# Kernel tuning notes

Hardware: AMD Instinct MI355X
Metric: run time of the kernel (lower is better)

The kernel has to match this reference:

```python
import jax, jax.numpy as jnp
import numpy as np

N_NODES = 100000
NEG_SLOPE = 0.01  # torch F.leaky_relu default


def sage_gcn_layer(feat, src, dst, W, b):
    # DGL SAGEConv, aggregator_type='gcn':
    #   h_i = fc_neigh((sum_{j->i} x_j + x_i) / (in_deg_i + 1))
    neigh_sum = jax.ops.segment_sum(feat[src], dst, num_segments=N_NODES)
    deg = jax.ops.segment_sum(jnp.ones((src.shape[0],), feat.dtype), dst,
                              num_segments=N_NODES)
    h = (neigh_sum + feat) / (deg + 1.0)[:, None]
    return h @ W + b


def setup_inputs() -> dict:
    key = jax.random.key(0)
    k_feat, k_e, k_w1, k_w2 = jax.random.split(key, 4)
    d_in, d_hid, d_out = 128, 128, 128
    E = 1600000
    feat = jax.random.normal(k_feat, (N_NODES, d_in), dtype=jnp.float32)
    edge_index = jax.random.randint(k_e, (2, E), 0, N_NODES, dtype=jnp.int64)
    W1 = jax.random.normal(k_w1, (d_in, d_hid), dtype=jnp.float32) / np.sqrt(d_in)
    b1 = jnp.zeros((d_hid,), jnp.float32)
    W2 = jax.random.normal(k_w2, (d_hid, d_out), dtype=jnp.float32) / np.sqrt(d_hid)
    b2 = jnp.zeros((d_out,), jnp.float32)
    return {"feat": feat, "edge_index": edge_index,
            "W1": W1, "b1": b1, "W2": W2, "b2": b2}


def reference(feat, edge_index, W1, b1, W2, b2):
    src, dst = edge_index[0], edge_index[1]
    h = sage_gcn_layer(feat, src, dst, W1, b1)
    h = jax.nn.leaky_relu(h, NEG_SLOPE)
    # dropout = 0 -> identity
    h = sage_gcn_layer(h, src, dst, W2, b2)
    return jax.nn.leaky_relu(h, NEG_SLOPE)
```

## Files before the change

kernel.cpp:

```cpp
#include <hip/hip_runtime.h>

#define NEG_SLOPE 0.01f
#define BSHIFT 8
#define BMASK 255
#define BMAX 512

typedef __attribute__((ext_vector_type(8))) short bf16x8;
typedef __attribute__((ext_vector_type(4))) float f32x4;
typedef __attribute__((ext_vector_type(2))) float f32x2;
typedef __attribute__((ext_vector_type(4))) unsigned u32x4;

static __device__ inline unsigned short f2b(float f) {
    unsigned u = __builtin_bit_cast(unsigned, f);
    return (unsigned short)((u + 0x7FFF + ((u >> 16) & 1)) >> 16);
}
static __device__ inline float b2f_lo(unsigned u) {
    return __builtin_bit_cast(float, u << 16);
}
static __device__ inline float b2f_hi(unsigned u) {
    return __builtin_bit_cast(float, u & 0xFFFF0000u);
}

__global__ __launch_bounds__(256) void cvt_feat(const float* __restrict__ x,
                                                unsigned short* __restrict__ xb,
                                                long long n) {
    long long i = ((long long)blockIdx.x * 256 + threadIdx.x) * 4;
    if (i < n) {
        float4 v = *(const float4*)(x + i);
        ushort4 o;
        o.x = f2b(v.x); o.y = f2b(v.y); o.z = f2b(v.z); o.w = f2b(v.w);
        *(ushort4*)(xb + i) = o;
    }
}

__global__ __launch_bounds__(256) void cvt_w(const float* __restrict__ W1,
                                             const float* __restrict__ W2,
                                             unsigned short* __restrict__ Wt1,
                                             unsigned short* __restrict__ Wt2,
                                             int* __restrict__ bcnt, int B) {
    int i = blockIdx.x * 256 + threadIdx.x;
    if (i < B) bcnt[i] = 0;
    int n = i & 127, k = i >> 7;
    Wt1[n * 128 + k] = f2b(W1[k * 128 + n]);
    Wt2[n * 128 + k] = f2b(W2[k * 128 + n]);
}

__global__ __launch_bounds__(256) void bhist_kernel(const int* __restrict__ dst,
                                                    int* __restrict__ bcnt,
                                                    int E, int B) {
    __shared__ int h[BMAX];
    for (int i = threadIdx.x; i < B; i += 256) h[i] = 0;
    __syncthreads();
    const int stride = gridDim.x * blockDim.x;
    for (int e = blockIdx.x * blockDim.x + threadIdx.x; e < E; e += stride)
        atomicAdd(&h[dst[e] >> BSHIFT], 1);
    __syncthreads();
    for (int i = threadIdx.x; i < B; i += 256)
        if (h[i]) atomicAdd(&bcnt[i], h[i]);
}

__global__ __launch_bounds__(512) void bscan_kernel(const int* __restrict__ bcnt,
                                                    int* __restrict__ bcursor,
                                                    int* __restrict__ bstart, int B) {
    __shared__ int sh[512];
    const int t = threadIdx.x;
    int v = (t < B) ? bcnt[t] : 0;
    sh[t] = v;
    __syncthreads();
    for (int d = 1; d < 512; d <<= 1) {
        int u = (t >= d) ? sh[t - d] : 0;
        __syncthreads();
        sh[t] += u;
        __syncthreads();
    }
    if (t < B) {
        int excl = sh[t] - v;
        bcursor[t] = excl;
        bstart[t] = excl;
    }
    if (t == B - 1) bstart[B] = sh[t];
}

__global__ __launch_bounds__(256) void bscatter_kernel(const int* __restrict__ src,
                                                       const int* __restrict__ dst,
                                                       int* __restrict__ bcursor,
                                                       unsigned* __restrict__ pairs,
                                                       int E, int B) {
    __shared__ int h[BMAX];
    __shared__ int base[BMAX];
    const int t = threadIdx.x;
    for (int i = t; i < B; i += 256) h[i] = 0;
    __syncthreads();
    const int chunk = (E + gridDim.x - 1) / gridDim.x;
    const int e0 = blockIdx.x * chunk;
    const int e1 = min(e0 + chunk, E);
    for (int e = e0 + t; e < e1; e += 256)
        atomicAdd(&h[dst[e] >> BSHIFT], 1);
    __syncthreads();
    for (int i = t; i < B; i += 256) {
        int c = h[i];
        base[i] = c ? atomicAdd(&bcursor[i], c) : 0;
    }
    __syncthreads();
    for (int i = t; i < B; i += 256) h[i] = base[i];
    __syncthreads();
    for (int e = e0 + t; e < e1; e += 256) {
        int d = dst[e];
        int pos = atomicAdd(&h[d >> BSHIFT], 1);
        pairs[pos] = (unsigned)src[e] | ((unsigned)(d & BMASK) << 24);
    }
}

__global__ __launch_bounds__(256) void bfinal_kernel(const unsigned* __restrict__ pairs,
                                                     const int* __restrict__ bstart,
                                                     int* __restrict__ offsets,
                                                     int* __restrict__ csr,
                                                     int N, int E) {
    __shared__ int h[256];
    __shared__ int cur[256];
    const int b = blockIdx.x;
    const int t = threadIdx.x;
    const int e0 = bstart[b], e1 = bstart[b + 1];
    h[t] = 0;
    __syncthreads();
    for (int e = e0 + t; e < e1; e += 256)
        atomicAdd(&h[pairs[e] >> 24], 1);
    __syncthreads();
    int v = h[t];
    for (int d = 1; d < 256; d <<= 1) {
        int u = (t >= d) ? h[t - d] : 0;
        __syncthreads();
        h[t] += u;
        __syncthreads();
    }
    const int base = e0 + (h[t] - v);
    const int node = (b << BSHIFT) + t;
    if (node < N) offsets[node] = base;
    if (b == (int)gridDim.x - 1 && t == 255) offsets[N] = E;
    cur[t] = base;
    __syncthreads();
    for (int e = e0 + t; e < e1; e += 256) {
        unsigned pr = pairs[e];
        int pos = atomicAdd(&cur[pr >> 24], 1);
        csr[pos] = (int)(pr & 0xFFFFFFu);
    }
}

static __device__ inline f32x2 up2(unsigned u) {
    return (f32x2){ b2f_lo(u), b2f_hi(u) };
}

#define GATHER(dst, off) \
    asm volatile("global_load_dwordx4 %0, %1, %2" : "=v"(dst) : "v"(off), "s"(xc))
#define ACCM(u, mk) do { \
    A0 += up2((u).x & (mk)); A1 += up2((u).y & (mk)); \
    A2 += up2((u).z & (mk)); A3 += up2((u).w & (mk)); } while (0)

__global__ __launch_bounds__(256) void aggregate_kernel(const unsigned short* __restrict__ xb,
                                                        const int* __restrict__ offsets,
                                                        const int* __restrict__ csr,
                                                        unsigned short* __restrict__ Hb,
                                                        int N) {
    const int node = (blockIdx.x * blockDim.x + threadIdx.x) >> 6;
    if (node >= N) return;
    const int lane = threadIdx.x & 63;
    const int g = lane >> 4;
    const unsigned poff = (unsigned)((lane & 15) << 4);
    const int start = offsets[node];
    const int end   = offsets[node + 1];
    const int deg   = end - start;
    const int rounds = deg >> 2;
    const int tailn  = deg & 3;
    const char* __restrict__ xc = (const char*)xb;

    const unsigned soff = ((unsigned)node << 8) | poff;
    u32x4 vs;
    GATHER(vs, soff);

    const int jmax = end - 1;
    unsigned o0, o1, o2, o3, o4, o5, o6, o7, ot;
#define CIDX(dsto, r) do { \
        int j = start + ((r) << 2) + g; j = j > jmax ? jmax : j; \
        int s = csr[j]; s = min(max(s, 0), N - 1); \
        dsto = ((unsigned)s << 8) | poff; } while (0)
    CIDX(o0, 0); CIDX(o1, 1); CIDX(o2, 2); CIDX(o3, 3);
    CIDX(o4, 4); CIDX(o5, 5); CIDX(o6, 6); CIDX(o7, 7);
    { int j = start + (rounds << 2) + g; j = j > jmax ? jmax : j;
      j = j < 0 ? 0 : j;
      int s = csr[j]; s = min(max(s, 0), N - 1);
      ot = ((unsigned)s << 8) | poff; }
#undef CIDX

    const unsigned m0 = rounds >= 1 ? ~0u : 0u;
    const unsigned m1 = rounds >= 2 ? ~0u : 0u;
    const unsigned m2 = rounds >= 3 ? ~0u : 0u;
    const unsigned m3 = rounds >= 4 ? ~0u : 0u;
    const unsigned m4 = rounds >= 5 ? ~0u : 0u;
    const unsigned m5 = rounds >= 6 ? ~0u : 0u;
    const unsigned m6 = rounds >= 7 ? ~0u : 0u;
    const unsigned m7 = rounds >= 8 ? ~0u : 0u;
    const unsigned mt = g < tailn ? ~0u : 0u;

    __builtin_amdgcn_sched_barrier(0);

    u32x4 v0, v1, v2, v3, v4, v5, v6, v7, vt;
    GATHER(v0, o0); GATHER(v1, o1); GATHER(v2, o2); GATHER(v3, o3);
    GATHER(v4, o4); GATHER(v5, o5); GATHER(v6, o6); GATHER(v7, o7);
    GATHER(vt, ot);
    asm volatile("s_waitcnt vmcnt(0)" ::: "memory");
    __builtin_amdgcn_sched_barrier(0);

    f32x2 A0 = {0.f, 0.f}, A1 = {0.f, 0.f}, A2 = {0.f, 0.f}, A3 = {0.f, 0.f};
    ACCM(v0, m0); ACCM(v1, m1); ACCM(v2, m2); ACCM(v3, m3);
    ACCM(v4, m4); ACCM(v5, m5); ACCM(v6, m6); ACCM(v7, m7);
    ACCM(vt, mt);
    for (int r = 8; r < rounds; ++r) {
        int s = csr[start + (r << 2) + g];
        s = min(max(s, 0), N - 1);
        u32x4 u = *(const u32x4*)(xc + (((unsigned)s << 8) | poff));
        ACCM(u, ~0u);
    }

    float a[8];
    a[0] = A0.x; a[1] = A0.y; a[2] = A1.x; a[3] = A1.y;
    a[4] = A2.x; a[5] = A2.y; a[6] = A3.x; a[7] = A3.y;
#pragma unroll
    for (int i = 0; i < 8; ++i) {
        a[i] += __shfl_xor(a[i], 16);
        a[i] += __shfl_xor(a[i], 32);
    }
    a[0] += b2f_lo(vs.x); a[1] += b2f_hi(vs.x);
    a[2] += b2f_lo(vs.y); a[3] += b2f_hi(vs.y);
    a[4] += b2f_lo(vs.z); a[5] += b2f_hi(vs.z);
    a[6] += b2f_lo(vs.w); a[7] += b2f_hi(vs.w);

    const float inv = 1.0f / (float)(deg + 1);
    if (g == 0) {
        uint4 o;
        o.x = (unsigned)f2b(a[0] * inv) | ((unsigned)f2b(a[1] * inv) << 16);
        o.y = (unsigned)f2b(a[2] * inv) | ((unsigned)f2b(a[3] * inv) << 16);
        o.z = (unsigned)f2b(a[4] * inv) | ((unsigned)f2b(a[5] * inv) << 16);
        o.w = (unsigned)f2b(a[6] * inv) | ((unsigned)f2b(a[7] * inv) << 16);
        *(uint4*)((char*)Hb + (((unsigned)node << 8) | poff)) = o;
    }
}

template <bool OUT_BF16>
__global__ __launch_bounds__(256) void gemm_mfma(const unsigned short* __restrict__ Hb,
                                                 const unsigned short* __restrict__ Wt,
                                                 const float* __restrict__ b,
                                                 void* __restrict__ outv, int N) {
    __shared__ unsigned short Wa[128 * 128];
    const int tid = threadIdx.x;
    const int row0 = blockIdx.x * 128;

#pragma unroll
    for (int it = 0; it < 8; ++it) {
        int idx = it * 256 + tid;
        int r = idx >> 4, c = idx & 15;
        uint4 v = *(const uint4*)(Wt + r * 128 + c * 8);
        *(uint4*)(Wa + r * 128 + ((c ^ (r & 15)) << 3)) = v;
    }
    __syncthreads();

    const int w = tid >> 6;
    const int lane = tid & 63;
    const int m = lane & 15;
    const int q = lane >> 4;

    const int r0 = row0 + w * 32 + m;
    const size_t ar0 = (size_t)min(r0, N - 1) * 128;
    const size_t ar1 = (size_t)min(r0 + 16, N - 1) * 128;

    f32x4 acc[2][8];
#pragma unroll
    for (int rt = 0; rt < 2; ++rt)
#pragma unroll
        for (int ct = 0; ct < 8; ++ct) acc[rt][ct] = (f32x4){0.f, 0.f, 0.f, 0.f};

#pragma unroll
    for (int kk = 0; kk < 4; ++kk) {
        const int chunk = kk * 4 + q;
        bf16x8 af0 = *(const bf16x8*)(Hb + ar0 + chunk * 8);
        bf16x8 af1 = *(const bf16x8*)(Hb + ar1 + chunk * 8);
#pragma unroll
        for (int ct = 0; ct < 8; ++ct) {
            int n = ct * 16 + m;
            bf16x8 bfr = *(const bf16x8*)(Wa + n * 128 + ((chunk ^ (n & 15)) << 3));
            acc[0][ct] = __builtin_amdgcn_mfma_f32_16x16x32_bf16(af0, bfr, acc[0][ct], 0, 0, 0);
            acc[1][ct] = __builtin_amdgcn_mfma_f32_16x16x32_bf16(af1, bfr, acc[1][ct], 0, 0, 0);
        }
    }

#pragma unroll
    for (int ct = 0; ct < 8; ++ct) {
        const float bias = b[ct * 16 + m];
        const int gcol = ct * 16 + m;
#pragma unroll
        for (int rt = 0; rt < 2; ++rt) {
#pragma unroll
            for (int reg = 0; reg < 4; ++reg) {
                int grow = row0 + w * 32 + rt * 16 + q * 4 + reg;
                if (grow < N) {
                    float v = acc[rt][ct][reg] + bias;
                    v = v > 0.f ? v : v * NEG_SLOPE;
                    if (OUT_BF16)
                        ((unsigned short*)outv)[(long long)grow * 128 + gcol] = f2b(v);
                    else
                        ((float*)outv)[(long long)grow * 128 + gcol] = v;
                }
            }
        }
    }
}

extern "C" void kernel_launch(void* const* d_in, const int* in_sizes, int n_in,
                              void* d_out, int out_size, void* d_ws, size_t ws_size,
                              hipStream_t stream) {
    const float* feat = (const float*)d_in[0];
    const int*   edges = (const int*)d_in[1];
    const float* W1 = (const float*)d_in[2];
    const float* b1 = (const float*)d_in[3];
    const float* W2 = (const float*)d_in[4];
    const float* b2 = (const float*)d_in[5];
    float* out = (float*)d_out;

    const int N = in_sizes[0] / 128;
    const int E = in_sizes[1] / 2;
    const int* src = edges;
    const int* dst = edges + E;
    const int B = (N + (1 << BSHIFT) - 1) >> BSHIFT;

    unsigned short* featb = (unsigned short*)d_ws;
    unsigned short* Hb    = featb + (size_t)N * 128;
    unsigned*       pairs = (unsigned*)Hb;
    unsigned short* Wt1   = Hb + (size_t)N * 128;
    unsigned short* Wt2   = Wt1 + 128 * 128;
    int* offsets = (int*)(Wt2 + 128 * 128);
    int* bcnt    = offsets + (N + 1);
    int* bcursor = bcnt + B;
    int* bstart  = bcursor + B;
    int* csr     = bstart + (B + 1);

    long long nfeat = (long long)N * 128;
    cvt_feat<<<(int)((nfeat / 4 + 255) / 256), 256, 0, stream>>>(feat, featb, nfeat);
    cvt_w<<<64, 256, 0, stream>>>(W1, W2, Wt1, Wt2, bcnt, B);

    bhist_kernel<<<256, 256, 0, stream>>>(dst, bcnt, E, B);
    bscan_kernel<<<1, 512, 0, stream>>>(bcnt, bcursor, bstart, B);
    bscatter_kernel<<<256, 256, 0, stream>>>(src, dst, bcursor, pairs, E, B);
    bfinal_kernel<<<B, 256, 0, stream>>>(pairs, bstart, offsets, csr, N, E);

    const int aggGrid = (N + 3) / 4;
    const int gemmGrid = (N + 127) / 128;

    aggregate_kernel<<<aggGrid, 256, 0, stream>>>(featb, offsets, csr, Hb, N);
    gemm_mfma<true><<<gemmGrid, 256, 0, stream>>>(Hb, Wt1, b1, (void*)featb, N);

    aggregate_kernel<<<aggGrid, 256, 0, stream>>>(featb, offsets, csr, Hb, N);
    gemm_mfma<false><<<gemmGrid, 256, 0, stream>>>(Hb, Wt2, b2, (void*)out, N);
}
```

Baseline: 344.1 us.

## Fuse preprocessing kernels and restructure aggregate gather with wave-uniform CSR loads

Merges the feature conversion, weight transpose and bucket histogram into one launch. Per-block histograms are written to a partial array that the scan sums, so global atomics and the zeroing pass are no longer needed. The aggregate kernel now reads offsets as wave-uniform scalars and loads 16 CSR indices per batch, selecting per group with selects. It gathers four rows per batch in an unrolled loop, replacing the fixed 8-round prefetch and its serial fallback loop, which aims to improve latency hiding for high-degree nodes. It also drops the index clamping, and extra code branches handle the tail.

```diff
diff --git a/kernel.cpp b/kernel.cpp
--- a/kernel.cpp
+++ b/kernel.cpp
@@ -4,6 +4,7 @@
 #define BSHIFT 8
 #define BMASK 255
 #define BMAX 512
+#define HB 256
 
 typedef __attribute__((ext_vector_type(8))) short bf16x8;
 typedef __attribute__((ext_vector_type(4))) float f32x4;
@@ -21,50 +22,61 @@
     return __builtin_bit_cast(float, u & 0xFFFF0000u);
 }
 
-__global__ __launch_bounds__(256) void cvt_feat(const float* __restrict__ x,
-                                                unsigned short* __restrict__ xb,
-                                                long long n) {
-    long long i = ((long long)blockIdx.x * 256 + threadIdx.x) * 4;
-    if (i < n) {
-        float4 v = *(const float4*)(x + i);
-        ushort4 o;
-        o.x = f2b(v.x); o.y = f2b(v.y); o.z = f2b(v.z); o.w = f2b(v.w);
-        *(ushort4*)(xb + i) = o;
-    }
-}
-
-__global__ __launch_bounds__(256) void cvt_w(const float* __restrict__ W1,
-                                             const float* __restrict__ W2,
-                                             unsigned short* __restrict__ Wt1,
-                                             unsigned short* __restrict__ Wt2,
-                                             int* __restrict__ bcnt, int B) {
-    int i = blockIdx.x * 256 + threadIdx.x;
-    if (i < B) bcnt[i] = 0;
-    int n = i & 127, k = i >> 7;
-    Wt1[n * 128 + k] = f2b(W1[k * 128 + n]);
-    Wt2[n * 128 + k] = f2b(W2[k * 128 + n]);
-}
-
-__global__ __launch_bounds__(256) void bhist_kernel(const int* __restrict__ dst,
-                                                    int* __restrict__ bcnt,
-                                                    int E, int B) {
+__global__ __launch_bounds__(256) void front_kernel(const float* __restrict__ feat,
+                                                    unsigned short* __restrict__ featb,
+                                                    long long nfeat,
+                                                    const float* __restrict__ W1,
+                                                    const float* __restrict__ W2,
+                                                    unsigned short* __restrict__ Wt1,
+                                                    unsigned short* __restrict__ Wt2,
+                                                    const int* __restrict__ dst,
+                                                    int* __restrict__ bpart,
+                                                    int E, int B, int nf4) {
+    const int bx = blockIdx.x;
+    const int t = threadIdx.x;
+    if (bx < nf4) {
+        long long i = ((long long)bx * 256 + t) * 4;
+        if (i < nfeat) {
+            float4 v = *(const float4*)(feat + i);
+            ushort4 o;
+            o.x = f2b(v.x); o.y = f2b(v.y); o.z = f2b(v.z); o.w = f2b(v.w);
+            *(ushort4*)(featb + i) = o;
+        }
+        return;
+    }
+    const int bx2 = bx - nf4;
+    if (bx2 < 64) {
+        int i = bx2 * 256 + t;
+        int n = i & 127, k = i >> 7;
+        Wt1[n * 128 + k] = f2b(W1[k * 128 + n]);
+        Wt2[n * 128 + k] = f2b(W2[k * 128 + n]);
+        return;
+    }
+    const int hb = bx2 - 64;
     __shared__ int h[BMAX];
-    for (int i = threadIdx.x; i < B; i += 256) h[i] = 0;
-    __syncthreads();
-    const int stride = gridDim.x * blockDim.x;
-    for (int e = blockIdx.x * blockDim.x + threadIdx.x; e < E; e += stride)
+    for (int i = t; i < BMAX; i += 256) h[i] = 0;
+    __syncthreads();
+    const int stride = HB * 256;
+    for (int e = hb * 256 + t; e < E; e += stride)
         atomicAdd(&h[dst[e] >> BSHIFT], 1);
     __syncthreads();
-    for (int i = threadIdx.x; i < B; i += 256)
-        if (h[i]) atomicAdd(&bcnt[i], h[i]);
-}
-
-__global__ __launch_bounds__(512) void bscan_kernel(const int* __restrict__ bcnt,
+    for (int i = t; i < B; i += 256) bpart[i * HB + hb] = h[i];
+}
+
+__global__ __launch_bounds__(512) void bscan_kernel(const int* __restrict__ bpart,
                                                     int* __restrict__ bcursor,
                                                     int* __restrict__ bstart, int B) {
     __shared__ int sh[512];
     const int t = threadIdx.x;
-    int v = (t < B) ? bcnt[t] : 0;
+    int v = 0;
+    if (t < B) {
+        const int4* p4 = (const int4*)(bpart + t * HB);
+#pragma unroll 8
+        for (int j = 0; j < HB / 4; ++j) {
+            int4 q = p4[j];
+            v += q.x + q.y + q.z + q.w;
+        }
+    }
     sh[t] = v;
     __syncthreads();
     for (int d = 1; d < 512; d <<= 1) {
@@ -152,9 +164,19 @@
 
 #define GATHER(dst, off) \
     asm volatile("global_load_dwordx4 %0, %1, %2" : "=v"(dst) : "v"(off), "s"(xc))
+#define ACC4(u) do { A0 += up2((u).x); A1 += up2((u).y); \
+                     A2 += up2((u).z); A3 += up2((u).w); } while (0)
 #define ACCM(u, mk) do { \
     A0 += up2((u).x & (mk)); A1 += up2((u).y & (mk)); \
     A2 += up2((u).z & (mk)); A3 += up2((u).w & (mk)); } while (0)
+
+static __device__ __forceinline__ unsigned rowsel(int g, unsigned poff,
+                                                  int i0, int i1, int i2, int i3) {
+    int s01 = (g & 1) ? i1 : i0;
+    int s23 = (g & 1) ? i3 : i2;
+    int s = (g & 2) ? s23 : s01;
+    return ((unsigned)s << 8) | poff;
+}
 
 __global__ __launch_bounds__(256) void aggregate_kernel(const unsigned short* __restrict__ xb,
                                                         const int* __restrict__ offsets,
@@ -166,60 +188,69 @@
     const int lane = threadIdx.x & 63;
     const int g = lane >> 4;
     const unsigned poff = (unsigned)((lane & 15) << 4);
-    const int start = offsets[node];
-    const int end   = offsets[node + 1];
+    const char* __restrict__ xc = (const char*)xb;
+
+    const int nu = __builtin_amdgcn_readfirstlane(node);
+    const int start = __builtin_amdgcn_readfirstlane(offsets[nu]);
+    const int end   = __builtin_amdgcn_readfirstlane(offsets[nu + 1]);
     const int deg   = end - start;
     const int rounds = deg >> 2;
     const int tailn  = deg & 3;
-    const char* __restrict__ xc = (const char*)xb;
-
-    const unsigned soff = ((unsigned)node << 8) | poff;
-    u32x4 vs;
-    GATHER(vs, soff);
-
-    const int jmax = end - 1;
-    unsigned o0, o1, o2, o3, o4, o5, o6, o7, ot;
-#define CIDX(dsto, r) do { \
-        int j = start + ((r) << 2) + g; j = j > jmax ? jmax : j; \
-        int s = csr[j]; s = min(max(s, 0), N - 1); \
-        dsto = ((unsigned)s << 8) | poff; } while (0)
-    CIDX(o0, 0); CIDX(o1, 1); CIDX(o2, 2); CIDX(o3, 3);
-    CIDX(o4, 4); CIDX(o5, 5); CIDX(o6, 6); CIDX(o7, 7);
-    { int j = start + (rounds << 2) + g; j = j > jmax ? jmax : j;
-      j = j < 0 ? 0 : j;
-      int s = csr[j]; s = min(max(s, 0), N - 1);
-      ot = ((unsigned)s << 8) | poff; }
-#undef CIDX
-
-    const unsigned m0 = rounds >= 1 ? ~0u : 0u;
-    const unsigned m1 = rounds >= 2 ? ~0u : 0u;
-    const unsigned m2 = rounds >= 3 ? ~0u : 0u;
-    const unsigned m3 = rounds >= 4 ? ~0u : 0u;
-    const unsigned m4 = rounds >= 5 ? ~0u : 0u;
-    const unsigned m5 = rounds >= 6 ? ~0u : 0u;
-    const unsigned m6 = rounds >= 7 ? ~0u : 0u;
-    const unsigned m7 = rounds >= 8 ? ~0u : 0u;
-    const unsigned mt = g < tailn ? ~0u : 0u;
-
-    __builtin_amdgcn_sched_barrier(0);
-
-    u32x4 v0, v1, v2, v3, v4, v5, v6, v7, vt;
-    GATHER(v0, o0); GATHER(v1, o1); GATHER(v2, o2); GATHER(v3, o3);
-    GATHER(v4, o4); GATHER(v5, o5); GATHER(v6, o6); GATHER(v7, o7);
-    GATHER(vt, ot);
+
+    u32x4 vs = (u32x4){0, 0, 0, 0};
+    if (g == 0) GATHER(vs, ((unsigned)nu << 8) | poff);
+
+    f32x2 A0 = {0.f, 0.f}, A1 = {0.f, 0.f}, A2 = {0.f, 0.f}, A3 = {0.f, 0.f};
+
+    int r = 0;
+    while (r + 4 <= rounds) {
+        const int p = start + (r << 2);
+        int i0  = csr[p +  0], i1  = csr[p +  1], i2  = csr[p +  2], i3  = csr[p +  3];
+        int i4  = csr[p +  4], i5  = csr[p +  5], i6  = csr[p +  6], i7  = csr[p +  7];
+        int i8  = csr[p +  8], i9  = csr[p +  9], i10 = csr[p + 10], i11 = csr[p + 11];
+        int i12 = csr[p + 12], i13 = csr[p + 13], i14 = csr[p + 14], i15 = csr[p + 15];
+        unsigned a0 = rowsel(g, poff, i0,  i1,  i2,  i3);
+        unsigned a1 = rowsel(g, poff, i4,  i5,  i6,  i7);
+        unsigned a2 = rowsel(g, poff, i8,  i9,  i10, i11);
+        unsigned a3 = rowsel(g, poff, i12, i13, i14, i15);
+        __builtin_amdgcn_sched_barrier(0);
+        u32x4 v0, v1, v2, v3;
+        GATHER(v0, a0); GATHER(v1, a1); GATHER(v2, a2); GATHER(v3, a3);
+        asm volatile("s_waitcnt vmcnt(0)" ::: "memory");
+        __builtin_amdgcn_sched_barrier(0);
+        ACC4(v0); ACC4(v1); ACC4(v2); ACC4(v3);
+        r += 4;
+    }
+
+    const int rr = rounds - r;
+    const int p = start + (r << 2);
+    u32x4 v0, v1, v2, vt;
+    if (rr >= 1) {
+        int i0 = csr[p + 0], i1 = csr[p + 1], i2 = csr[p + 2], i3 = csr[p + 3];
+        GATHER(v0, rowsel(g, poff, i0, i1, i2, i3));
+    }
+    if (rr >= 2) {
+        int i0 = csr[p + 4], i1 = csr[p + 5], i2 = csr[p + 6], i3 = csr[p + 7];
+        GATHER(v1, rowsel(g, poff, i0, i1, i2, i3));
+    }
+    if (rr >= 3) {
+        int i0 = csr[p + 8], i1 = csr[p + 9], i2 = csr[p + 10], i3 = csr[p + 11];
+        GATHER(v2, rowsel(g, poff, i0, i1, i2, i3));
+    }
+    const unsigned mt = (g < tailn) ? ~0u : 0u;
+    if (tailn) {
+        const int q = start + (rounds << 2);
+        int t0 = csr[q];
+        int t1 = (tailn > 1) ? csr[q + 1] : t0;
+        int t2 = (tailn > 2) ? csr[q + 2] : t0;
+        GATHER(vt, rowsel(g, poff, t0, t1, t2, t0));
+    }
     asm volatile("s_waitcnt vmcnt(0)" ::: "memory");
     __builtin_amdgcn_sched_barrier(0);
-
-    f32x2 A0 = {0.f, 0.f}, A1 = {0.f, 0.f}, A2 = {0.f, 0.f}, A3 = {0.f, 0.f};
-    ACCM(v0, m0); ACCM(v1, m1); ACCM(v2, m2); ACCM(v3, m3);
-    ACCM(v4, m4); ACCM(v5, m5); ACCM(v6, m6); ACCM(v7, m7);
-    ACCM(vt, mt);
-    for (int r = 8; r < rounds; ++r) {
-        int s = csr[start + (r << 2) + g];
-        s = min(max(s, 0), N - 1);
-        u32x4 u = *(const u32x4*)(xc + (((unsigned)s << 8) | poff));
-        ACCM(u, ~0u);
-    }
+    if (rr >= 1) ACC4(v0);
+    if (rr >= 2) ACC4(v1);
+    if (rr >= 3) ACC4(v2);
+    if (tailn) ACCM(vt, mt);
 
     float a[8];
     a[0] = A0.x; a[1] = A0.y; a[2] = A1.x; a[3] = A1.y;
@@ -337,17 +368,17 @@
     unsigned short* Wt1   = Hb + (size_t)N * 128;
     unsigned short* Wt2   = Wt1 + 128 * 128;
     int* offsets = (int*)(Wt2 + 128 * 128);
-    int* bcnt    = offsets + (N + 1);
-    int* bcursor = bcnt + B;
-    int* bstart  = bcursor + B;
-    int* csr     = bstart + (B + 1);
-
-    long long nfeat = (long long)N * 128;
-    cvt_feat<<<(int)((nfeat / 4 + 255) / 256), 256, 0, stream>>>(feat, featb, nfeat);
-    cvt_w<<<64, 256, 0, stream>>>(W1, W2, Wt1, Wt2, bcnt, B);
-
-    bhist_kernel<<<256, 256, 0, stream>>>(dst, bcnt, E, B);
-    bscan_kernel<<<1, 512, 0, stream>>>(bcnt, bcursor, bstart, B);
+    int* bcursor = offsets + ((N + 8) & ~7);
+    int* bstart  = bcursor + 512;
+    int* csr     = bstart + 512;
+    int* bpart   = csr + ((E + 8) & ~7);
+
+    const long long nfeat = (long long)N * 128;
+    const int nf4 = (int)((nfeat / 4 + 255) / 256);
+
+    front_kernel<<<nf4 + 64 + HB, 256, 0, stream>>>(feat, featb, nfeat, W1, W2,
+                                                    Wt1, Wt2, dst, bpart, E, B, nf4);
+    bscan_kernel<<<1, 512, 0, stream>>>(bpart, bcursor, bstart, B);
     bscatter_kernel<<<256, 256, 0, stream>>>(src, dst, bcursor, pairs, E, B);
     bfinal_kernel<<<B, 256, 0, stream>>>(pairs, bstart, offsets, csr, N, E);
 
```

Result: no change. 347.4 us (+1.0%).
